# Optimization experiments

Hardware: AMD Instinct MI355X
Metric: run time of the kernel (lower is better)

## Reference

```python
import jax, jax.numpy as jnp
import numpy as np

B, N, E, H = 8, 512, 256, 8
HD = E // H
FF = 4 * E
TOPK = max(1, int(N * 0.2))
FW_MAX_DIST = 10      # default of get_shortest_path_matrix
EMB_MAX_IDX = 6       # spd encoder: max_dist(5) + 1
LN_EPS = 1e-5


def _layernorm(x, g, b):
    m = jnp.mean(x, axis=-1, keepdims=True)
    v = jnp.var(x, axis=-1, keepdims=True)
    return (x - m) / jnp.sqrt(v + LN_EPS) * g + b


def setup_inputs() -> dict:
    key = jax.random.key(0)
    ks = jax.random.split(key, 12)
    s = 0.02
    return {
        "x": jax.random.normal(ks[0], (B, N, E), jnp.float32),
        "adj": jax.random.uniform(ks[1], (B, N, N), jnp.float32),
        "emb_spd": (jax.random.normal(ks[2], (EMB_MAX_IDX + 1, H), jnp.float32) * s),
        "w_qkv": jax.random.normal(ks[3], (3 * E, E), jnp.float32) * s,
        "b_qkv": jnp.zeros((3 * E,), jnp.float32),
        "w_out": jax.random.normal(ks[4], (E, E), jnp.float32) * s,
        "b_out": jnp.zeros((E,), jnp.float32),
        "w_ff1": jax.random.normal(ks[5], (FF, E), jnp.float32) * s,
        "b_ff1": jnp.zeros((FF,), jnp.float32),
        "w_ff2": jax.random.normal(ks[6], (E, FF), jnp.float32) * s,
        "b_ff2": jnp.zeros((E,), jnp.float32),
        "g1": jnp.ones((E,), jnp.float32),
        "beta1": jnp.zeros((E,), jnp.float32),
        "g2": jnp.ones((E,), jnp.float32),
        "beta2": jnp.zeros((E,), jnp.float32),
        "w_pool": jax.random.normal(ks[7], (1, E), jnp.float32) * s,
        "b_pool": jnp.zeros((1,), jnp.float32),
    }


def _combined_mask(adj, emb_spd):
    # top-k per row -> binary adjacency via scatter
    _, idx = jax.lax.top_k(adj, TOPK)                       # [B,N,k]
    bi = jnp.arange(B)[:, None, None]
    ri = jnp.arange(N)[None, :, None]
    binary = jnp.zeros_like(adj).at[bi, ri, idx].set(1.0)   # [B,N,N]

    # Floyd-Warshall shortest paths
    dist = jnp.where(binary == 1.0, 1.0, jnp.inf)
    ids = jnp.arange(N)
    dist = dist.at[:, ids, ids].set(0.0)

    def body(k, d):
        return jnp.minimum(d, d[:, :, k][:, :, None] + d[:, k, :][:, None, :])

    dist = jax.lax.fori_loop(0, N, body, dist)
    dist_i = jnp.where(dist > FW_MAX_DIST, -1.0, dist).astype(jnp.int32)

    # spatial bias embedding: indices = clamp(dist+1, 0, max_dist+1)
    sp_idx = jnp.clip(dist_i + 1, 0, EMB_MAX_IDX)           # [B,N,N]
    bias = jnp.transpose(emb_spd[sp_idx], (0, 3, 1, 2))     # [B,H,N,N]

    base = jnp.where(binary == 0.0, -jnp.inf, 0.0)[:, None] # [B,1,N,N]
    return base + bias                                      # [B,H,N,N]


def reference(x, adj, emb_spd, w_qkv, b_qkv, w_out, b_out,
              w_ff1, b_ff1, w_ff2, b_ff2, g1, beta1, g2, beta2,
              w_pool, b_pool):
    mask = _combined_mask(adj, emb_spd)                     # [B,H,N,N]

    # multi-head self-attention (PyTorch MHA, post-norm encoder layer, eval)
    qkv = x @ w_qkv.T + b_qkv                               # [B,N,3E]
    q, k, v = jnp.split(qkv, 3, axis=-1)
    q = q.reshape(B, N, H, HD).transpose(0, 2, 1, 3)
    k = k.reshape(B, N, H, HD).transpose(0, 2, 1, 3)
    v = v.reshape(B, N, H, HD).transpose(0, 2, 1, 3)
    scores = jnp.einsum("bhqd,bhkd->bhqk", q, k) / np.sqrt(HD) + mask
    attn = jax.nn.softmax(scores, axis=-1)
    ctx = jnp.einsum("bhqk,bhkd->bhqd", attn, v)
    ctx = ctx.transpose(0, 2, 1, 3).reshape(B, N, E)
    attn_out = ctx @ w_out.T + b_out

    x1 = _layernorm(x + attn_out, g1, beta1)
    ff = jax.nn.relu(x1 @ w_ff1.T + b_ff1) @ w_ff2.T + b_ff2
    x2 = _layernorm(x1 + ff, g2, beta2)

    # attention pooling over nodes
    w = jax.nn.softmax(jnp.tanh(x2 @ w_pool.T + b_pool), axis=1)  # [B,N,1]
    return jnp.sum(x2 * w, axis=1)                          # [B,E]
```

## Files before the change

### kernel.cpp

```cpp
#include <hip/hip_runtime.h>
#include <math.h>


#define B_ 8
#define N_ 512
#define E_ 256
#define H_ 8
#define HD_ 32
#define TOPK_ 102

typedef __attribute__((ext_vector_type(8))) short bf16x8;
typedef __attribute__((ext_vector_type(4))) float f32x4;

__device__ __forceinline__ unsigned short f2b(float f) {
  unsigned u = __builtin_bit_cast(unsigned, f);
  return (unsigned short)((u + 0x7FFFu + ((u >> 16) & 1u)) >> 16);
}

__global__ __launch_bounds__(256) void cvt_all(
    const float* __restrict__ x, const float* __restrict__ wqkv,
    const float* __restrict__ wout, const float* __restrict__ wff1,
    const float* __restrict__ wff2, unsigned short* __restrict__ xb,
    unsigned short* __restrict__ wqkvb, unsigned short* __restrict__ woutb,
    unsigned short* __restrict__ wff1b, unsigned short* __restrict__ wff2b) {
  int i = (blockIdx.x * 256 + threadIdx.x) * 4;
  const float* src;
  unsigned short* dst;
  int off;
  if (i < 1048576)      { src = x;    dst = xb;    off = i; }
  else if (i < 1245184) { src = wqkv; dst = wqkvb; off = i - 1048576; }
  else if (i < 1310720) { src = wout; dst = woutb; off = i - 1245184; }
  else if (i < 1572864) { src = wff1; dst = wff1b; off = i - 1310720; }
  else                  { src = wff2; dst = wff2b; off = i - 1572864; }
  float4 v = *(const float4*)(src + off);
  ushort4 o;
  o.x = f2b(v.x); o.y = f2b(v.y); o.z = f2b(v.z); o.w = f2b(v.w);
  *(ushort4*)(dst + off) = o;
}

__global__ __launch_bounds__(256) void topk_kernel(const float* __restrict__ adj,
                                                   unsigned int* __restrict__ bits) {
  const int row = blockIdx.x;
  const float* a = adj + (size_t)row * N_;
  __shared__ unsigned int hist[1024];
  __shared__ float cval[N_];
  __shared__ int cidx[N_];
  __shared__ int s_cnt;
  __shared__ int s_bb;
  __shared__ int s_need;
  __shared__ unsigned int rowbits[16];
  __shared__ int wsum[4];
  const int t = threadIdx.x;
  const int lane = t & 63;
  const int wave = t >> 6;

  hist[t] = 0u; hist[t + 256] = 0u; hist[t + 512] = 0u; hist[t + 768] = 0u;
  if (t == 0) s_cnt = 0;
  float v0 = a[t];
  float v1 = a[t + 256];
  __syncthreads();
  const int b0 = min(1023, max(0, (int)(v0 * 1024.0f)));
  const int b1 = min(1023, max(0, (int)(v1 * 1024.0f)));
  atomicAdd(&hist[b0], 1u);
  atomicAdd(&hist[b1], 1u);
  __syncthreads();
  const int base = 1020 - 4 * t;
  const int h0 = (int)hist[base], h1 = (int)hist[base + 1];
  const int h2 = (int)hist[base + 2], h3 = (int)hist[base + 3];
  const int g = h0 + h1 + h2 + h3;
  int sc = g;
  #pragma unroll
  for (int off = 1; off < 64; off <<= 1) {
    int y = __shfl_up(sc, off);
    sc += (lane >= off) ? y : 0;
  }
  if (lane == 63) wsum[wave] = sc;
  __syncthreads();
  int wo = 0;
  for (int w = 0; w < wave; w++) wo += wsum[w];
  const int incl = sc + wo;
  const int excl = incl - g;
  if (excl < TOPK_ && incl >= TOPK_) {
    int cum = excl;
    int bb = base;
    const int hh[4] = {h3, h2, h1, h0};
    const int bs[4] = {base + 3, base + 2, base + 1, base};
    #pragma unroll
    for (int u = 0; u < 4; u++) {
      if (cum + hh[u] >= TOPK_) { bb = bs[u]; break; }
      cum += hh[u];
    }
    s_bb = bb;
    s_need = TOPK_ - cum;
  }
  __syncthreads();
  const int bb = s_bb;
  const int need = s_need;
  const bool sel0 = (b0 > bb);
  const bool sel1 = (b1 > bb);
  if (b0 == bb) { int p = atomicAdd(&s_cnt, 1); cval[p] = v0; cidx[p] = t; }
  if (b1 == bb) { int p = atomicAdd(&s_cnt, 1); cval[p] = v1; cidx[p] = t + 256; }
  unsigned long long m0 = __ballot(sel0);
  unsigned long long m1 = __ballot(sel1);
  if (lane == 0) {
    rowbits[2 * wave + 0] = (unsigned int)m0;
    rowbits[2 * wave + 1] = (unsigned int)(m0 >> 32);
    rowbits[8 + 2 * wave + 0] = (unsigned int)m1;
    rowbits[8 + 2 * wave + 1] = (unsigned int)(m1 >> 32);
  }
  __syncthreads();
  const int cnt = s_cnt;
  for (int c = t; c < cnt; c += 256) {
    const float v = cval[c];
    const int idx = cidx[c];
    int r = 0;
    for (int j = 0; j < cnt; j++) {
      const float vj = cval[j];
      const int ij = cidx[j];
      if (vj > v || (vj == v && ij < idx)) r++;
    }
    if (r < need) atomicOr(&rowbits[idx >> 5], 1u << (idx & 31));
  }
  __syncthreads();
  if (t < 16) bits[(size_t)row * 16 + t] = rowbits[t];
}

__global__ __launch_bounds__(256) void gemm_mfma(
    const unsigned short* __restrict__ A, const unsigned short* __restrict__ W,
    const float* __restrict__ bias, const float* __restrict__ res,
    void* __restrict__ Cout, unsigned short* __restrict__ kG,
    unsigned short* __restrict__ vG, int M, int N, int K, int flags) {
  __shared__ __align__(16) unsigned short Af[8 * 64 * 8];
  __shared__ __align__(16) unsigned short Wf[8 * 64 * 8];
  const int tid = threadIdx.x;
  const int m0 = blockIdx.y * 64, n0 = blockIdx.x * 64;
  const int wave = tid >> 6, lane = tid & 63;
  const int wm = wave & 1, wn = wave >> 1;
  const int q = lane >> 4, l15 = lane & 15;
  const int r = tid >> 2, c0 = tid & 3;

  f32x4 acc[2][2];
  #pragma unroll
  for (int i = 0; i < 2; i++)
    #pragma unroll
    for (int j = 0; j < 2; j++) acc[i][j] = (f32x4){0.f, 0.f, 0.f, 0.f};

  const size_t arow = (size_t)(m0 + r) * K;
  const size_t wrow = (size_t)(n0 + r) * K;
  for (int k0 = 0; k0 < K; k0 += 64) {
    uint4 a0 = *(const uint4*)(A + arow + k0 + c0 * 8);
    uint4 a1 = *(const uint4*)(A + arow + k0 + (c0 + 4) * 8);
    uint4 w0 = *(const uint4*)(W + wrow + k0 + c0 * 8);
    uint4 w1 = *(const uint4*)(W + wrow + k0 + (c0 + 4) * 8);
    __syncthreads();
    {
      int kc = c0 >> 2, qq = c0 & 3;
      int s0 = ((r >> 4) * 2 + kc) * 64 + (r & 15) + qq * 16;
      int kc1 = (c0 + 4) >> 2, qq1 = (c0 + 4) & 3;
      int s1 = ((r >> 4) * 2 + kc1) * 64 + (r & 15) + qq1 * 16;
      *(uint4*)(Af + s0 * 8) = a0;
      *(uint4*)(Af + s1 * 8) = a1;
      *(uint4*)(Wf + s0 * 8) = w0;
      *(uint4*)(Wf + s1 * 8) = w1;
    }
    __syncthreads();
    #pragma unroll
    for (int kc = 0; kc < 2; kc++) {
      bf16x8 af[2], wf[2];
      #pragma unroll
      for (int mt = 0; mt < 2; mt++)
        af[mt] = *(const bf16x8*)(Af + (((wm * 2 + mt) * 2 + kc) * 64 + lane) * 8);
      #pragma unroll
      for (int nt = 0; nt < 2; nt++)
        wf[nt] = *(const bf16x8*)(Wf + (((wn * 2 + nt) * 2 + kc) * 64 + lane) * 8);
      #pragma unroll
      for (int mt = 0; mt < 2; mt++)
        #pragma unroll
        for (int nt = 0; nt < 2; nt++)
          acc[mt][nt] = __builtin_amdgcn_mfma_f32_16x16x32_bf16(af[mt], wf[nt], acc[mt][nt], 0, 0, 0);
    }
  }
  #pragma unroll
  for (int nt = 0; nt < 2; nt++) {
    const int col = n0 + (wn * 2 + nt) * 16 + l15;
    const float bv = bias[col];
    #pragma unroll
    for (int mt = 0; mt < 2; mt++) {
      const int rowb = m0 + (wm * 2 + mt) * 16 + q * 4;
      float ov[4];
      #pragma unroll
      for (int reg = 0; reg < 4; reg++) {
        float o = acc[mt][nt][reg] + bv;
        if (res) o += res[(size_t)(rowb + reg) * N + col];
        if (flags & 1) o = fmaxf(o, 0.f);
        ov[reg] = o;
      }
      if (kG && col >= 256 && col < 512) {
        const int dfull = col - 256;
        const int hh2 = dfull >> 5, d = dfull & 31;
        const int q2 = d >> 3, sub = d & 7;
        const int bidx = rowb >> 9, j = rowb & 511;
        const int jt = j >> 6, jtile = (j >> 4) & 3, jl = j & 15;
        unsigned short* kp = kG +
            ((size_t)(((bidx * 8 + hh2) * 8 + jt) * 4 + jtile) * 64 + q2 * 16 + jl) * 8 + sub;
        kp[0] = f2b(ov[0]); kp[8] = f2b(ov[1]); kp[16] = f2b(ov[2]); kp[24] = f2b(ov[3]);
      } else if (vG && col >= 512) {
        const int dfull = col - 512;
        const int hh2 = dfull >> 5, d = dfull & 31;
        const int dt = d >> 4, dl = d & 15;
        const int bidx = rowb >> 9, j = rowb & 511;
        const int jt = j >> 6, jj = j & 63;
        const int kc = jj >> 5, q2 = (jj >> 3) & 3, sub0 = jj & 7;
        ushort4 st;
        st.x = f2b(ov[0]); st.y = f2b(ov[1]); st.z = f2b(ov[2]); st.w = f2b(ov[3]);
        *(ushort4*)(vG +
            ((size_t)(((bidx * 8 + hh2) * 8 + jt) * 4 + dt * 2 + kc) * 64 + q2 * 16 + dl) * 8 + sub0) = st;
      } else {
        #pragma unroll
        for (int reg = 0; reg < 4; reg++) {
          if (flags & 2) ((unsigned short*)Cout)[(size_t)(rowb + reg) * N + col] = f2b(ov[reg]);
          else           ((float*)Cout)[(size_t)(rowb + reg) * N + col] = ov[reg];
        }
      }
    }
  }
}

__global__ __launch_bounds__(256) void attn_mfma(
    const unsigned short* __restrict__ qkv, const unsigned short* __restrict__ kG,
    const unsigned short* __restrict__ vG, const unsigned int* __restrict__ bits,
    const float* __restrict__ emb, unsigned short* __restrict__ ctxo) {
  const int bx = blockIdx.x;
  const int ib = bx & 7;
  const int h = (bx >> 3) & 7;
  const int b = bx >> 6;
  const int tid = threadIdx.x;
  const int lane = tid & 63;
  const int wave = tid >> 6;
  const int q = lane >> 4, l15 = lane & 15;

  __shared__ __align__(16) unsigned int mrow[64 * 16];
  __shared__ __align__(16) unsigned short pF[4][2 * 64 * 8];

  {
    int rr = tid >> 2, wq = tid & 3;
    uint4 mw = *(const uint4*)(bits + ((size_t)(b * N_ + ib * 64 + rr)) * 16 + wq * 4);
    *(uint4*)(mrow + rr * 16 + wq * 4) = mw;
  }
  __syncthreads();

  const int i0w = ib * 64 + wave * 16;
  const bf16x8 qf = *(const bf16x8*)(qkv + ((size_t)(b * N_ + i0w + l15)) * 768 + h * HD_ + q * 8);
  const float delta = emb[1 * H_ + h] - emb[2 * H_ + h];
  const float scale = 0.17677669529663687f;

  float m_run[4], l_run[4];
  #pragma unroll
  for (int e = 0; e < 4; e++) { m_run[e] = -1e30f; l_run[e] = 0.f; }
  f32x4 cacc[2];
  cacc[0] = (f32x4){0.f, 0.f, 0.f, 0.f};
  cacc[1] = (f32x4){0.f, 0.f, 0.f, 0.f};

  unsigned short* pbase = &pF[wave][0];
  const unsigned short* kb = kG + (size_t)(b * 8 + h) * 8 * 4 * 512;
  const unsigned short* vb = vG + (size_t)(b * 8 + h) * 8 * 4 * 512;

  #pragma unroll 1
  for (int jt = 0; jt < 8; jt++) {
    f32x4 s4[4];
    #pragma unroll
    for (int jtile = 0; jtile < 4; jtile++) {
      bf16x8 kf = *(const bf16x8*)(kb + (size_t)(jt * 4 + jtile) * 512 + lane * 8);
      s4[jtile] = __builtin_amdgcn_mfma_f32_16x16x32_bf16(qf, kf, (f32x4){0.f, 0.f, 0.f, 0.f}, 0, 0, 0);
    }
    unsigned long long mw64[4];
    #pragma unroll
    for (int reg = 0; reg < 4; reg++)
      mw64[reg] = *(const unsigned long long*)(mrow + (wave * 16 + q * 4 + reg) * 16 + jt * 2);
    float smat[4][4];
    #pragma unroll
    for (int jtile = 0; jtile < 4; jtile++) {
      #pragma unroll
      for (int reg = 0; reg < 4; reg++) {
        unsigned int w = (jtile & 2) ? (unsigned int)(mw64[reg] >> 32) : (unsigned int)mw64[reg];
        bool allowed = ((w >> ((jtile & 1) * 16 + l15)) & 1u) != 0u;
        int ig = ib * 64 + wave * 16 + q * 4 + reg;
        int jg = jt * 64 + jtile * 16 + l15;
        float s = s4[jtile][reg] * scale + ((jg == ig) ? delta : 0.f);
        smat[jtile][reg] = allowed ? s : -INFINITY;
      }
    }
    float alpha[4], pmat[4][4];
    #pragma unroll
    for (int reg = 0; reg < 4; reg++) {
      float mloc = fmaxf(fmaxf(smat[0][reg], smat[1][reg]), fmaxf(smat[2][reg], smat[3][reg]));
      #pragma unroll
      for (int off = 1; off < 16; off <<= 1) mloc = fmaxf(mloc, __shfl_xor(mloc, off));
      float mnew = fmaxf(m_run[reg], mloc);
      alpha[reg] = __expf(m_run[reg] - mnew);
      m_run[reg] = mnew;
      float ps = 0.f;
      #pragma unroll
      for (int jtile = 0; jtile < 4; jtile++) {
        float p = __expf(smat[jtile][reg] - mnew);
        pmat[jtile][reg] = p;
        ps += p;
      }
      #pragma unroll
      for (int off = 1; off < 16; off <<= 1) ps += __shfl_xor(ps, off);
      l_run[reg] = l_run[reg] * alpha[reg] + ps;
      cacc[0][reg] *= alpha[reg];
      cacc[1][reg] *= alpha[reg];
    }
    #pragma unroll
    for (int jtile = 0; jtile < 4; jtile++) {
      int j_l = jtile * 16 + l15;
      int sl = ((j_l >> 5) * 64 + ((j_l >> 3) & 3) * 16) * 8 + (j_l & 7);
      #pragma unroll
      for (int reg = 0; reg < 4; reg++)
        pbase[sl + (q * 4 + reg) * 8] = f2b(pmat[jtile][reg]);
    }
    #pragma unroll
    for (int kc = 0; kc < 2; kc++) {
      bf16x8 pf = *(const bf16x8*)(pbase + (kc * 64 + lane) * 8);
      #pragma unroll
      for (int dt = 0; dt < 2; dt++) {
        bf16x8 vf = *(const bf16x8*)(vb + (size_t)(jt * 4 + dt * 2 + kc) * 512 + lane * 8);
        cacc[dt] = __builtin_amdgcn_mfma_f32_16x16x32_bf16(pf, vf, cacc[dt], 0, 0, 0);
      }
    }
  }
  #pragma unroll
  for (int reg = 0; reg < 4; reg++) {
    const float linv = 1.f / l_run[reg];
    const size_t row = (size_t)(b * N_ + i0w + q * 4 + reg);
    #pragma unroll
    for (int dt = 0; dt < 2; dt++)
      ctxo[row * E_ + h * HD_ + dt * 16 + l15] = f2b(cacc[dt][reg] * linv);
  }
}

__global__ __launch_bounds__(256) void layernorm_kernel(
    const float* __restrict__ t, const float* __restrict__ g,
    const float* __restrict__ be, float* __restrict__ out,
    unsigned short* __restrict__ outb, const float* __restrict__ wp,
    const float* __restrict__ bp, float* __restrict__ ew) {
  const int row = blockIdx.x;
  const int tid = threadIdx.x;
  float v = t[(size_t)row * E_ + tid];
  float s = v, s2 = v * v;
  #pragma unroll
  for (int off = 32; off > 0; off >>= 1) {
    s += __shfl_xor(s, off);
    s2 += __shfl_xor(s2, off);
  }
  __shared__ float sh[8];
  const int wave = tid >> 6, lane = tid & 63;
  if (lane == 0) { sh[wave] = s; sh[4 + wave] = s2; }
  __syncthreads();
  s = sh[0] + sh[1] + sh[2] + sh[3];
  s2 = sh[4] + sh[5] + sh[6] + sh[7];
  float mean = s * (1.f / 256.f);
  float var = s2 * (1.f / 256.f) - mean * mean;
  float inv = rsqrtf(var + 1e-5f);
  float o = (v - mean) * inv * g[tid] + be[tid];
  out[(size_t)row * E_ + tid] = o;
  if (outb) outb[(size_t)row * E_ + tid] = f2b(o);
  if (ew) {
    float d = o * wp[tid];
    #pragma unroll
    for (int off = 32; off > 0; off >>= 1) d += __shfl_xor(d, off);
    __syncthreads();
    if (lane == 0) sh[wave] = d;
    __syncthreads();
    if (tid == 0) {
      float dot = sh[0] + sh[1] + sh[2] + sh[3] + bp[0];
      ew[row] = __expf(tanhf(dot));
    }
  }
}

__global__ __launch_bounds__(256) void pool_partial(
    const float* __restrict__ x2, const float* __restrict__ ew,
    float* __restrict__ partial, float* __restrict__ pwsum) {
  const int c = blockIdx.x;
  const int b = blockIdx.y;
  const int tid = threadIdx.x;
  const int r0 = b * N_ + c * 16;
  float acc = 0.f;
  #pragma unroll
  for (int n = 0; n < 16; n++)
    acc += ew[r0 + n] * x2[(size_t)(r0 + n) * E_ + tid];
  partial[(size_t)(b * 32 + c) * E_ + tid] = acc;
  if (tid < 16) {
    float w = ew[r0 + tid];
    #pragma unroll
    for (int off = 1; off < 16; off <<= 1) w += __shfl_xor(w, off);
    if (tid == 0) pwsum[b * 32 + c] = w;
  }
}

__global__ __launch_bounds__(256) void pool_final(
    const float* __restrict__ partial, const float* __restrict__ pwsum,
    float* __restrict__ out) {
  const int b = blockIdx.x;
  const int tid = threadIdx.x;
  float acc = 0.f, ws = 0.f;
  #pragma unroll
  for (int c = 0; c < 32; c++) acc += partial[(size_t)(b * 32 + c) * E_ + tid];
  #pragma unroll
  for (int c = 0; c < 32; c++) ws += pwsum[b * 32 + c];
  out[b * E_ + tid] = acc / ws;
}

extern "C" void kernel_launch(void* const* d_in, const int* in_sizes, int n_in,
                              void* d_out, int out_size, void* d_ws, size_t ws_size,
                              hipStream_t stream) {
  (void)in_sizes; (void)n_in; (void)out_size; (void)ws_size;
  const float* x      = (const float*)d_in[0];
  const float* adj    = (const float*)d_in[1];
  const float* emb    = (const float*)d_in[2];
  const float* w_qkv  = (const float*)d_in[3];
  const float* b_qkv  = (const float*)d_in[4];
  const float* w_out  = (const float*)d_in[5];
  const float* b_out  = (const float*)d_in[6];
  const float* w_ff1  = (const float*)d_in[7];
  const float* b_ff1  = (const float*)d_in[8];
  const float* w_ff2  = (const float*)d_in[9];
  const float* b_ff2  = (const float*)d_in[10];
  const float* g1     = (const float*)d_in[11];
  const float* be1    = (const float*)d_in[12];
  const float* g2     = (const float*)d_in[13];
  const float* be2    = (const float*)d_in[14];
  const float* w_pool = (const float*)d_in[15];
  const float* b_pool = (const float*)d_in[16];

  char* ws = (char*)d_ws;
  unsigned int*   bits  = (unsigned int*)ws;
  unsigned short* xb    = (unsigned short*)(ws + 262144);
  unsigned short* qkvb  = (unsigned short*)(ws + 2359296);
  unsigned short* hffb  = xb;
  unsigned short* ctxb  = (unsigned short*)(ws + 8650752);
  unsigned short* x1b   = (unsigned short*)(ws + 10747904);
  unsigned short* wqkvb = (unsigned short*)(ws + 12845056);
  unsigned short* woutb = (unsigned short*)(ws + 13238272);
  unsigned short* wff1b = (unsigned short*)(ws + 13369344);
  unsigned short* wff2b = (unsigned short*)(ws + 13893632);
  unsigned short* vG    = (unsigned short*)(ws + 14417920);
  unsigned short* kG    = (unsigned short*)(ws + 16515072);
  float*          tbuf  = (float*)(ws + 18612224);
  float*          x1    = (float*)(ws + 22806528);
  float*          x2    = (float*)(ws + 27000832);
  float*          ew      = (float*)(ws + 8650752);
  float*          partial = (float*)(ws + 8650752 + 16384);
  float*          pwsum   = (float*)(ws + 8650752 + 16384 + 262144);
  float*          outp  = (float*)d_out;

  const int M = B_ * N_;

  cvt_all<<<1835008 / 1024, 256, 0, stream>>>(x, w_qkv, w_out, w_ff1, w_ff2,
                                              xb, wqkvb, woutb, wff1b, wff2b);
  topk_kernel<<<B_ * N_, 256, 0, stream>>>(adj, bits);
  gemm_mfma<<<dim3(768 / 64, M / 64), 256, 0, stream>>>(
      xb, wqkvb, b_qkv, nullptr, qkvb, kG, vG, M, 768, E_, 2);
  attn_mfma<<<B_ * H_ * (N_ / 64), 256, 0, stream>>>(qkvb, kG, vG, bits, emb, ctxb);
  gemm_mfma<<<dim3(E_ / 64, M / 64), 256, 0, stream>>>(
      ctxb, woutb, b_out, x, tbuf, nullptr, nullptr, M, E_, E_, 0);
  layernorm_kernel<<<M, 256, 0, stream>>>(tbuf, g1, be1, x1, x1b,
                                          nullptr, nullptr, nullptr);
  gemm_mfma<<<dim3(1024 / 64, M / 64), 256, 0, stream>>>(
      x1b, wff1b, b_ff1, nullptr, hffb, nullptr, nullptr, M, 1024, E_, 1 | 2);
  gemm_mfma<<<dim3(E_ / 64, M / 64), 256, 0, stream>>>(
      hffb, wff2b, b_ff2, x1, tbuf, nullptr, nullptr, M, E_, 1024, 0);
  layernorm_kernel<<<M, 256, 0, stream>>>(tbuf, g2, be2, x2, nullptr,
                                          w_pool, b_pool, ew);
  pool_partial<<<dim3(32, 8), 256, 0, stream>>>(x2, ew, partial, pwsum);
  pool_final<<<B_, 256, 0, stream>>>(partial, pwsum, outp);
}
```

Measured before the change: 177.5 us.

## Fuse transformer stages into cooperative persistent megakernel with grid syncs

```diff
diff --git a/kernel.cpp b/kernel.cpp
--- a/kernel.cpp
+++ b/kernel.cpp
@@ -1,4 +1,5 @@
 #include <hip/hip_runtime.h>
+#include <hip/hip_cooperative_groups.h>
 #include <math.h>
 
 
@@ -9,6 +10,8 @@
 #define HD_ 32
 #define TOPK_ 102
 
+namespace cg = cooperative_groups;
+
 typedef __attribute__((ext_vector_type(8))) short bf16x8;
 typedef __attribute__((ext_vector_type(4))) float f32x4;
 
@@ -17,40 +20,53 @@
   return (unsigned short)((u + 0x7FFFu + ((u >> 16) & 1u)) >> 16);
 }
 
-__global__ __launch_bounds__(256) void cvt_all(
+struct SmemGemm { unsigned short Af[8 * 64 * 8]; unsigned short Wf[8 * 64 * 8]; };
+struct SmemAttn { unsigned int mrow[64 * 16]; unsigned short pF[4][2 * 64 * 8]; };
+struct SmemLN   { float red[8]; };
+union SmemU { SmemGemm gm; SmemAttn at; SmemLN ln; };
+
+struct MegaArgs {
+  const unsigned short *xb, *wqkvb, *woutb, *wff1b, *wff2b;
+  const unsigned int* bits;
+  const float *x, *emb, *b_qkv, *b_out, *b_ff1, *b_ff2;
+  const float *g1, *be1, *g2, *be2, *wp, *bp;
+  unsigned short *qb, *kG, *vG, *ctxb, *x1b, *hffb;
+  float *tbuf, *x1, *partial, *pwsum, *outp;
+};
+
+__global__ __launch_bounds__(256) void cvt_topk(
+    const float* __restrict__ adj, unsigned int* __restrict__ bits,
     const float* __restrict__ x, const float* __restrict__ wqkv,
     const float* __restrict__ wout, const float* __restrict__ wff1,
     const float* __restrict__ wff2, unsigned short* __restrict__ xb,
     unsigned short* __restrict__ wqkvb, unsigned short* __restrict__ woutb,
     unsigned short* __restrict__ wff1b, unsigned short* __restrict__ wff2b) {
-  int i = (blockIdx.x * 256 + threadIdx.x) * 4;
-  const float* src;
-  unsigned short* dst;
-  int off;
-  if (i < 1048576)      { src = x;    dst = xb;    off = i; }
-  else if (i < 1245184) { src = wqkv; dst = wqkvb; off = i - 1048576; }
-  else if (i < 1310720) { src = wout; dst = woutb; off = i - 1245184; }
-  else if (i < 1572864) { src = wff1; dst = wff1b; off = i - 1310720; }
-  else                  { src = wff2; dst = wff2b; off = i - 1572864; }
-  float4 v = *(const float4*)(src + off);
-  ushort4 o;
-  o.x = f2b(v.x); o.y = f2b(v.y); o.z = f2b(v.z); o.w = f2b(v.w);
-  *(ushort4*)(dst + off) = o;
-}
-
-__global__ __launch_bounds__(256) void topk_kernel(const float* __restrict__ adj,
-                                                   unsigned int* __restrict__ bits) {
-  const int row = blockIdx.x;
-  const float* a = adj + (size_t)row * N_;
   __shared__ unsigned int hist[1024];
-  __shared__ float cval[N_];
-  __shared__ int cidx[N_];
-  __shared__ int s_cnt;
-  __shared__ int s_bb;
-  __shared__ int s_need;
+  __shared__ float cval[64];
+  __shared__ int cidx[64];
+  __shared__ int s_cnt, s_bb, s_need;
   __shared__ unsigned int rowbits[16];
   __shared__ int wsum[4];
   const int t = threadIdx.x;
+
+  if (blockIdx.x >= 4096) {
+    int i = ((blockIdx.x - 4096) * 256 + t) * 4;
+    const float* src;
+    unsigned short* dst;
+    int off;
+    if (i < 1048576)      { src = x;    dst = xb;    off = i; }
+    else if (i < 1245184) { src = wqkv; dst = wqkvb; off = i - 1048576; }
+    else if (i < 1310720) { src = wout; dst = woutb; off = i - 1245184; }
+    else if (i < 1572864) { src = wff1; dst = wff1b; off = i - 1310720; }
+    else                  { src = wff2; dst = wff2b; off = i - 1572864; }
+    float4 v = *(const float4*)(src + off);
+    ushort4 o;
+    o.x = f2b(v.x); o.y = f2b(v.y); o.z = f2b(v.z); o.w = f2b(v.w);
+    *(ushort4*)(dst + off) = o;
+    return;
+  }
+  const int row = blockIdx.x;
+  const float* a = adj + (size_t)row * N_;
   const int lane = t & 63;
   const int wave = t >> 6;
 
@@ -98,8 +114,8 @@
   const int need = s_need;
   const bool sel0 = (b0 > bb);
   const bool sel1 = (b1 > bb);
-  if (b0 == bb) { int p = atomicAdd(&s_cnt, 1); cval[p] = v0; cidx[p] = t; }
-  if (b1 == bb) { int p = atomicAdd(&s_cnt, 1); cval[p] = v1; cidx[p] = t + 256; }
+  if (b0 == bb) { int p = atomicAdd(&s_cnt, 1); if (p < 64) { cval[p] = v0; cidx[p] = t; } }
+  if (b1 == bb) { int p = atomicAdd(&s_cnt, 1); if (p < 64) { cval[p] = v1; cidx[p] = t + 256; } }
   unsigned long long m0 = __ballot(sel0);
   unsigned long long m1 = __ballot(sel1);
   if (lane == 0) {
@@ -109,7 +125,7 @@
     rowbits[8 + 2 * wave + 1] = (unsigned int)(m1 >> 32);
   }
   __syncthreads();
-  const int cnt = s_cnt;
+  const int cnt = min(s_cnt, 64);
   for (int c = t; c < cnt; c += 256) {
     const float v = cval[c];
     const int idx = cidx[c];
@@ -125,15 +141,15 @@
   if (t < 16) bits[(size_t)row * 16 + t] = rowbits[t];
 }
 
-__global__ __launch_bounds__(256) void gemm_mfma(
+__device__ __forceinline__ void gemm_tile(
+    unsigned short* __restrict__ Af, unsigned short* __restrict__ Wf,
     const unsigned short* __restrict__ A, const unsigned short* __restrict__ W,
     const float* __restrict__ bias, const float* __restrict__ res,
-    void* __restrict__ Cout, unsigned short* __restrict__ kG,
-    unsigned short* __restrict__ vG, int M, int N, int K, int flags) {
-  __shared__ __align__(16) unsigned short Af[8 * 64 * 8];
-  __shared__ __align__(16) unsigned short Wf[8 * 64 * 8];
+    void* __restrict__ Cout, unsigned short* __restrict__ qb,
+    unsigned short* __restrict__ kG, unsigned short* __restrict__ vG,
+    int bx, int by, int N, int K, int flags) {
   const int tid = threadIdx.x;
-  const int m0 = blockIdx.y * 64, n0 = blockIdx.x * 64;
+  const int m0 = by * 64, n0 = bx * 64;
   const int wave = tid >> 6, lane = tid & 63;
   const int wm = wave & 1, wn = wave >> 1;
   const int q = lane >> 4, l15 = lane & 15;
@@ -195,42 +211,51 @@
         if (flags & 1) o = fmaxf(o, 0.f);
         ov[reg] = o;
       }
-      if (kG && col >= 256 && col < 512) {
-        const int dfull = col - 256;
-        const int hh2 = dfull >> 5, d = dfull & 31;
-        const int q2 = d >> 3, sub = d & 7;
-        const int bidx = rowb >> 9, j = rowb & 511;
-        const int jt = j >> 6, jtile = (j >> 4) & 3, jl = j & 15;
-        unsigned short* kp = kG +
-            ((size_t)(((bidx * 8 + hh2) * 8 + jt) * 4 + jtile) * 64 + q2 * 16 + jl) * 8 + sub;
-        kp[0] = f2b(ov[0]); kp[8] = f2b(ov[1]); kp[16] = f2b(ov[2]); kp[24] = f2b(ov[3]);
-      } else if (vG && col >= 512) {
-        const int dfull = col - 512;
-        const int hh2 = dfull >> 5, d = dfull & 31;
-        const int dt = d >> 4, dl = d & 15;
-        const int bidx = rowb >> 9, j = rowb & 511;
-        const int jt = j >> 6, jj = j & 63;
-        const int kc = jj >> 5, q2 = (jj >> 3) & 3, sub0 = jj & 7;
-        ushort4 st;
-        st.x = f2b(ov[0]); st.y = f2b(ov[1]); st.z = f2b(ov[2]); st.w = f2b(ov[3]);
-        *(ushort4*)(vG +
-            ((size_t)(((bidx * 8 + hh2) * 8 + jt) * 4 + dt * 2 + kc) * 64 + q2 * 16 + dl) * 8 + sub0) = st;
+      if (flags & 4) {
+        if (col < 256) {
+          #pragma unroll
+          for (int reg = 0; reg < 4; reg++)
+            qb[(size_t)(rowb + reg) * 256 + col] = f2b(ov[reg]);
+        } else if (col < 512) {
+          const int dfull = col - 256;
+          const int hh2 = dfull >> 5, d = dfull & 31;
+          const int q2 = d >> 3, sub = d & 7;
+          const int bidx = rowb >> 9, j = rowb & 511;
+          const int jt = j >> 6, jtile = (j >> 4) & 3, jl = j & 15;
+          unsigned short* kp = kG +
+              ((size_t)(((bidx * 8 + hh2) * 8 + jt) * 4 + jtile) * 64 + q2 * 16 + jl) * 8 + sub;
+          kp[0] = f2b(ov[0]); kp[8] = f2b(ov[1]); kp[16] = f2b(ov[2]); kp[24] = f2b(ov[3]);
+        } else {
+          const int dfull = col - 512;
+          const int hh2 = dfull >> 5, d = dfull & 31;
+          const int dt = d >> 4, dl = d & 15;
+          const int bidx = rowb >> 9, j = rowb & 511;
+          const int jt = j >> 6, jj = j & 63;
+          const int kc = jj >> 5, q2 = (jj >> 3) & 3, sub0 = jj & 7;
+          ushort4 st;
+          st.x = f2b(ov[0]); st.y = f2b(ov[1]); st.z = f2b(ov[2]); st.w = f2b(ov[3]);
+          *(ushort4*)(vG +
+              ((size_t)(((bidx * 8 + hh2) * 8 + jt) * 4 + dt * 2 + kc) * 64 + q2 * 16 + dl) * 8 + sub0) = st;
+        }
+      } else if (flags & 2) {
+        #pragma unroll
+        for (int reg = 0; reg < 4; reg++)
+          ((unsigned short*)Cout)[(size_t)(rowb + reg) * N + col] = f2b(ov[reg]);
       } else {
         #pragma unroll
-        for (int reg = 0; reg < 4; reg++) {
-          if (flags & 2) ((unsigned short*)Cout)[(size_t)(rowb + reg) * N + col] = f2b(ov[reg]);
-          else           ((float*)Cout)[(size_t)(rowb + reg) * N + col] = ov[reg];
-        }
+        for (int reg = 0; reg < 4; reg++)
+          ((float*)Cout)[(size_t)(rowb + reg) * N + col] = ov[reg];
       }
     }
   }
 }
 
-__global__ __launch_bounds__(256) void attn_mfma(
-    const unsigned short* __restrict__ qkv, const unsigned short* __restrict__ kG,
-    const unsigned short* __restrict__ vG, const unsigned int* __restrict__ bits,
-    const float* __restrict__ emb, unsigned short* __restrict__ ctxo) {
-  const int bx = blockIdx.x;
+__device__ __forceinline__ void attn_tile(
+    unsigned int* __restrict__ mrow, unsigned short* __restrict__ pFb,
+    int bx, const unsigned short* __restrict__ qbuf,
+    const unsigned short* __restrict__ kG, const unsigned short* __restrict__ vG,
+    const unsigned int* __restrict__ bits, const float* __restrict__ emb,
+    unsigned short* __restrict__ ctxo) {
   const int ib = bx & 7;
   const int h = (bx >> 3) & 7;
   const int b = bx >> 6;
@@ -239,9 +264,6 @@
   const int wave = tid >> 6;
   const int q = lane >> 4, l15 = lane & 15;
 
-  __shared__ __align__(16) unsigned int mrow[64 * 16];
-  __shared__ __align__(16) unsigned short pF[4][2 * 64 * 8];
-
   {
     int rr = tid >> 2, wq = tid & 3;
     uint4 mw = *(const uint4*)(bits + ((size_t)(b * N_ + ib * 64 + rr)) * 16 + wq * 4);
@@ -250,7 +272,7 @@
   __syncthreads();
 
   const int i0w = ib * 64 + wave * 16;
-  const bf16x8 qf = *(const bf16x8*)(qkv + ((size_t)(b * N_ + i0w + l15)) * 768 + h * HD_ + q * 8);
+  const bf16x8 qf = *(const bf16x8*)(qbuf + ((size_t)(b * N_ + i0w + l15)) * 256 + h * HD_ + q * 8);
   const float delta = emb[1 * H_ + h] - emb[2 * H_ + h];
   const float scale = 0.17677669529663687f;
 
@@ -261,7 +283,7 @@
   cacc[0] = (f32x4){0.f, 0.f, 0.f, 0.f};
   cacc[1] = (f32x4){0.f, 0.f, 0.f, 0.f};
 
-  unsigned short* pbase = &pF[wave][0];
+  unsigned short* pbase = pFb + wave * 1024;
   const unsigned short* kb = kG + (size_t)(b * 8 + h) * 8 * 4 * 512;
   const unsigned short* vb = vG + (size_t)(b * 8 + h) * 8 * 4 * 512;
 
@@ -340,77 +362,149 @@
   }
 }
 
-__global__ __launch_bounds__(256) void layernorm_kernel(
-    const float* __restrict__ t, const float* __restrict__ g,
-    const float* __restrict__ be, float* __restrict__ out,
-    unsigned short* __restrict__ outb, const float* __restrict__ wp,
-    const float* __restrict__ bp, float* __restrict__ ew) {
-  const int row = blockIdx.x;
+__device__ __forceinline__ void ln_row(
+    float* __restrict__ red, int row, const float* __restrict__ t,
+    const float* __restrict__ g, const float* __restrict__ be,
+    float* __restrict__ xo, unsigned short* __restrict__ xbo) {
   const int tid = threadIdx.x;
-  float v = t[(size_t)row * E_ + tid];
+  const int wave = tid >> 6, lane = tid & 63;
+  float v = t[(size_t)row * 256 + tid];
   float s = v, s2 = v * v;
   #pragma unroll
-  for (int off = 32; off > 0; off >>= 1) {
-    s += __shfl_xor(s, off);
-    s2 += __shfl_xor(s2, off);
-  }
-  __shared__ float sh[8];
-  const int wave = tid >> 6, lane = tid & 63;
-  if (lane == 0) { sh[wave] = s; sh[4 + wave] = s2; }
-  __syncthreads();
-  s = sh[0] + sh[1] + sh[2] + sh[3];
-  s2 = sh[4] + sh[5] + sh[6] + sh[7];
+  for (int off = 32; off > 0; off >>= 1) { s += __shfl_xor(s, off); s2 += __shfl_xor(s2, off); }
+  __syncthreads();
+  if (lane == 0) { red[wave] = s; red[4 + wave] = s2; }
+  __syncthreads();
+  s = red[0] + red[1] + red[2] + red[3];
+  s2 = red[4] + red[5] + red[6] + red[7];
   float mean = s * (1.f / 256.f);
   float var = s2 * (1.f / 256.f) - mean * mean;
   float inv = rsqrtf(var + 1e-5f);
   float o = (v - mean) * inv * g[tid] + be[tid];
-  out[(size_t)row * E_ + tid] = o;
-  if (outb) outb[(size_t)row * E_ + tid] = f2b(o);
-  if (ew) {
-    float d = o * wp[tid];
+  xo[(size_t)row * 256 + tid] = o;
+  xbo[(size_t)row * 256 + tid] = f2b(o);
+}
+
+__device__ __forceinline__ void ln2pool_chunk(
+    float* __restrict__ red, int c, const float* __restrict__ t,
+    const float* __restrict__ g, const float* __restrict__ be,
+    const float* __restrict__ wp, const float* __restrict__ bp,
+    float* __restrict__ partial, float* __restrict__ pwsum) {
+  const int tid = threadIdx.x;
+  const int wave = tid >> 6, lane = tid & 63;
+  const float wpv = wp[tid];
+  float pacc = 0.f, esum = 0.f;
+  #pragma unroll 1
+  for (int rr = 0; rr < 16; rr++) {
+    const int row = c * 16 + rr;
+    float v = t[(size_t)row * 256 + tid];
+    float s = v, s2 = v * v;
+    #pragma unroll
+    for (int off = 32; off > 0; off >>= 1) { s += __shfl_xor(s, off); s2 += __shfl_xor(s2, off); }
+    __syncthreads();
+    if (lane == 0) { red[wave] = s; red[4 + wave] = s2; }
+    __syncthreads();
+    s = red[0] + red[1] + red[2] + red[3];
+    s2 = red[4] + red[5] + red[6] + red[7];
+    float mean = s * (1.f / 256.f);
+    float var = s2 * (1.f / 256.f) - mean * mean;
+    float inv = rsqrtf(var + 1e-5f);
+    float o = (v - mean) * inv * g[tid] + be[tid];
+    float d = o * wpv;
     #pragma unroll
     for (int off = 32; off > 0; off >>= 1) d += __shfl_xor(d, off);
     __syncthreads();
-    if (lane == 0) sh[wave] = d;
+    if (lane == 0) red[wave] = d;
     __syncthreads();
-    if (tid == 0) {
-      float dot = sh[0] + sh[1] + sh[2] + sh[3] + bp[0];
-      ew[row] = __expf(tanhf(dot));
-    }
-  }
-}
-
-__global__ __launch_bounds__(256) void pool_partial(
-    const float* __restrict__ x2, const float* __restrict__ ew,
-    float* __restrict__ partial, float* __restrict__ pwsum) {
-  const int c = blockIdx.x;
-  const int b = blockIdx.y;
+    float dot = red[0] + red[1] + red[2] + red[3] + bp[0];
+    float e = __expf(tanhf(dot));
+    pacc += e * o;
+    esum += e;
+  }
+  partial[(size_t)c * 256 + tid] = pacc;
+  if (tid == 0) pwsum[c] = esum;
+}
+
+__device__ __forceinline__ void pool_final_task(
+    int b, const float* __restrict__ partial, const float* __restrict__ pwsum,
+    float* __restrict__ out) {
   const int tid = threadIdx.x;
-  const int r0 = b * N_ + c * 16;
-  float acc = 0.f;
-  #pragma unroll
-  for (int n = 0; n < 16; n++)
-    acc += ew[r0 + n] * x2[(size_t)(r0 + n) * E_ + tid];
-  partial[(size_t)(b * 32 + c) * E_ + tid] = acc;
-  if (tid < 16) {
-    float w = ew[r0 + tid];
-    #pragma unroll
-    for (int off = 1; off < 16; off <<= 1) w += __shfl_xor(w, off);
-    if (tid == 0) pwsum[b * 32 + c] = w;
-  }
-}
-
-__global__ __launch_bounds__(256) void pool_final(
-    const float* __restrict__ partial, const float* __restrict__ pwsum,
-    float* __restrict__ out) {
-  const int b = blockIdx.x;
-  const int tid = threadIdx.x;
-  float acc = 0.f, ws = 0.f;
-  #pragma unroll
-  for (int c = 0; c < 32; c++) acc += partial[(size_t)(b * 32 + c) * E_ + tid];
-  #pragma unroll
-  for (int c = 0; c < 32; c++) ws += pwsum[b * 32 + c];
-  out[b * E_ + tid] = acc / ws;
+  float acc = 0.f, wsv = 0.f;
+  #pragma unroll
+  for (int c = 0; c < 32; c++) acc += partial[(size_t)(b * 32 + c) * 256 + tid];
+  #pragma unroll
+  for (int c = 0; c < 32; c++) wsv += pwsum[b * 32 + c];
+  out[b * 256 + tid] = acc / wsv;
+}
+
+__global__ __launch_bounds__(256, 2) void mega(MegaArgs a) {
+  cg::grid_group gg = cg::this_grid();
+  __shared__ __align__(16) SmemU sm;
+  const int nb = gridDim.x, bid = blockIdx.x;
+
+  for (int t = bid; t < 768; t += nb)
+    gemm_tile(sm.gm.Af, sm.gm.Wf, a.xb, a.wqkvb, a.b_qkv, nullptr, nullptr,
+              a.qb, a.kG, a.vG, t % 12, t / 12, 768, 256, 4);
+  gg.sync();
+  for (int t = bid; t < 512; t += nb)
+    attn_tile(sm.at.mrow, &sm.at.pF[0][0], t, a.qb, a.kG, a.vG, a.bits, a.emb, a.ctxb);
+  gg.sync();
+  for (int t = bid; t < 256; t += nb)
+    gemm_tile(sm.gm.Af, sm.gm.Wf, a.ctxb, a.woutb, a.b_out, a.x, a.tbuf,
+              nullptr, nullptr, nullptr, t % 4, t / 4, 256, 256, 0);
+  gg.sync();
+  for (int rw = bid; rw < 4096; rw += nb)
+    ln_row(sm.ln.red, rw, a.tbuf, a.g1, a.be1, a.x1, a.x1b);
+  gg.sync();
+  for (int t = bid; t < 1024; t += nb)
+    gemm_tile(sm.gm.Af, sm.gm.Wf, a.x1b, a.wff1b, a.b_ff1, nullptr, a.hffb,
+              nullptr, nullptr, nullptr, t % 16, t / 16, 1024, 256, 1 | 2);
+  gg.sync();
+  for (int t = bid; t < 256; t += nb)
+    gemm_tile(sm.gm.Af, sm.gm.Wf, a.hffb, a.wff2b, a.b_ff2, a.x1, a.tbuf,
+              nullptr, nullptr, nullptr, t % 4, t / 4, 256, 1024, 0);
+  gg.sync();
+  for (int c = bid; c < 256; c += nb)
+    ln2pool_chunk(sm.ln.red, c, a.tbuf, a.g2, a.be2, a.wp, a.bp, a.partial, a.pwsum);
+  gg.sync();
+  for (int b = bid; b < 8; b += nb)
+    pool_final_task(b, a.partial, a.pwsum, a.outp);
+}
+
+__global__ __launch_bounds__(256) void k_qkv(MegaArgs a) {
+  __shared__ __align__(16) SmemGemm g;
+  gemm_tile(g.Af, g.Wf, a.xb, a.wqkvb, a.b_qkv, nullptr, nullptr, a.qb, a.kG, a.vG,
+            blockIdx.x, blockIdx.y, 768, 256, 4);
+}
+__global__ __launch_bounds__(256) void k_attn(MegaArgs a) {
+  __shared__ __align__(16) SmemAttn s;
+  attn_tile(s.mrow, &s.pF[0][0], blockIdx.x, a.qb, a.kG, a.vG, a.bits, a.emb, a.ctxb);
+}
+__global__ __launch_bounds__(256) void k_out(MegaArgs a) {
+  __shared__ __align__(16) SmemGemm g;
+  gemm_tile(g.Af, g.Wf, a.ctxb, a.woutb, a.b_out, a.x, a.tbuf, nullptr, nullptr, nullptr,
+            blockIdx.x, blockIdx.y, 256, 256, 0);
+}
+__global__ __launch_bounds__(256) void k_ln1(MegaArgs a) {
+  __shared__ float red[8];
+  ln_row(red, blockIdx.x, a.tbuf, a.g1, a.be1, a.x1, a.x1b);
+}
+__global__ __launch_bounds__(256) void k_ff1(MegaArgs a) {
+  __shared__ __align__(16) SmemGemm g;
+  gemm_tile(g.Af, g.Wf, a.x1b, a.wff1b, a.b_ff1, nullptr, a.hffb, nullptr, nullptr, nullptr,
+            blockIdx.x, blockIdx.y, 1024, 256, 1 | 2);
+}
+__global__ __launch_bounds__(256) void k_ff2(MegaArgs a) {
+  __shared__ __align__(16) SmemGemm g;
+  gemm_tile(g.Af, g.Wf, a.hffb, a.wff2b, a.b_ff2, a.x1, a.tbuf, nullptr, nullptr, nullptr,
+            blockIdx.x, blockIdx.y, 256, 1024, 0);
+}
+__global__ __launch_bounds__(256) void k_ln2pool(MegaArgs a) {
+  __shared__ float red[8];
+  ln2pool_chunk(red, blockIdx.x, a.tbuf, a.g2, a.be2, a.wp, a.bp, a.partial, a.pwsum);
+}
+__global__ __launch_bounds__(256) void k_poolfinal(MegaArgs a) {
+  pool_final_task(blockIdx.x, a.partial, a.pwsum, a.outp);
 }
 
 extern "C" void kernel_launch(void* const* d_in, const int* in_sizes, int n_in,
@@ -438,42 +532,46 @@
   char* ws = (char*)d_ws;
   unsigned int*   bits  = (unsigned int*)ws;
   unsigned short* xb    = (unsigned short*)(ws + 262144);
-  unsigned short* qkvb  = (unsigned short*)(ws + 2359296);
-  unsigned short* hffb  = xb;
+  unsigned short* qb    = (unsigned short*)(ws + 2359296);
+  unsigned short* kG    = (unsigned short*)(ws + 4456448);
+  unsigned short* vG    = (unsigned short*)(ws + 6553600);
   unsigned short* ctxb  = (unsigned short*)(ws + 8650752);
-  unsigned short* x1b   = (unsigned short*)(ws + 10747904);
-  unsigned short* wqkvb = (unsigned short*)(ws + 12845056);
-  unsigned short* woutb = (unsigned short*)(ws + 13238272);
-  unsigned short* wff1b = (unsigned short*)(ws + 13369344);
-  unsigned short* wff2b = (unsigned short*)(ws + 13893632);
-  unsigned short* vG    = (unsigned short*)(ws + 14417920);
-  unsigned short* kG    = (unsigned short*)(ws + 16515072);
-  float*          tbuf  = (float*)(ws + 18612224);
-  float*          x1    = (float*)(ws + 22806528);
-  float*          x2    = (float*)(ws + 27000832);
-  float*          ew      = (float*)(ws + 8650752);
-  float*          partial = (float*)(ws + 8650752 + 16384);
-  float*          pwsum   = (float*)(ws + 8650752 + 16384 + 262144);
+  float*          tbuf  = (float*)(ws + 10747904);
+  float*          x1    = (float*)(ws + 14942208);
+  unsigned short* x1b   = (unsigned short*)(ws + 19136512);
+  unsigned short* hffb  = (unsigned short*)(ws + 21233664);
+  unsigned short* wqkvb = (unsigned short*)(ws + 29622272);
+  unsigned short* woutb = (unsigned short*)(ws + 30015488);
+  unsigned short* wff1b = (unsigned short*)(ws + 30146560);
+  unsigned short* wff2b = (unsigned short*)(ws + 30670848);
+  float*          partial = (float*)(ws + 31195136);
+  float*          pwsum   = (float*)(ws + 31457280);
   float*          outp  = (float*)d_out;
 
-  const int M = B_ * N_;
-
-  cvt_all<<<1835008 / 1024, 256, 0, stream>>>(x, w_qkv, w_out, w_ff1, w_ff2,
-                                              xb, wqkvb, woutb, wff1b, wff2b);
-  topk_kernel<<<B_ * N_, 256, 0, stream>>>(adj, bits);
-  gemm_mfma<<<dim3(768 / 64, M / 64), 256, 0, stream>>>(
-      xb, wqkvb, b_qkv, nullptr, qkvb, kG, vG, M, 768, E_, 2);
-  attn_mfma<<<B_ * H_ * (N_ / 64), 256, 0, stream>>>(qkvb, kG, vG, bits, emb, ctxb);
-  gemm_mfma<<<dim3(E_ / 64, M / 64), 256, 0, stream>>>(
-      ctxb, woutb, b_out, x, tbuf, nullptr, nullptr, M, E_, E_, 0);
-  layernorm_kernel<<<M, 256, 0, stream>>>(tbuf, g1, be1, x1, x1b,
-                                          nullptr, nullptr, nullptr);
-  gemm_mfma<<<dim3(1024 / 64, M / 64), 256, 0, stream>>>(
-      x1b, wff1b, b_ff1, nullptr, hffb, nullptr, nullptr, M, 1024, E_, 1 | 2);
-  gemm_mfma<<<dim3(E_ / 64, M / 64), 256, 0, stream>>>(
-      hffb, wff2b, b_ff2, x1, tbuf, nullptr, nullptr, M, E_, 1024, 0);
-  layernorm_kernel<<<M, 256, 0, stream>>>(tbuf, g2, be2, x2, nullptr,
-                                          w_pool, b_pool, ew);
-  pool_partial<<<dim3(32, 8), 256, 0, stream>>>(x2, ew, partial, pwsum);
-  pool_final<<<B_, 256, 0, stream>>>(partial, pwsum, outp);
-}
+  cvt_topk<<<4096 + 1792, 256, 0, stream>>>(adj, bits, x, w_qkv, w_out, w_ff1,
+                                            w_ff2, xb, wqkvb, woutb, wff1b, wff2b);
+
+  MegaArgs ma;
+  ma.xb = xb; ma.wqkvb = wqkvb; ma.woutb = woutb; ma.wff1b = wff1b; ma.wff2b = wff2b;
+  ma.bits = bits;
+  ma.x = x; ma.emb = emb; ma.b_qkv = b_qkv; ma.b_out = b_out; ma.b_ff1 = b_ff1;
+  ma.b_ff2 = b_ff2; ma.g1 = g1; ma.be1 = be1; ma.g2 = g2; ma.be2 = be2;
+  ma.wp = w_pool; ma.bp = b_pool;
+  ma.qb = qb; ma.kG = kG; ma.vG = vG; ma.ctxb = ctxb; ma.x1b = x1b; ma.hffb = hffb;
+  ma.tbuf = tbuf; ma.x1 = x1; ma.partial = partial; ma.pwsum = pwsum; ma.outp = outp;
+
+  void* kp[] = {&ma};
+  hipError_t err = hipLaunchCooperativeKernel((void*)mega, dim3(512), dim3(256),
+                                              kp, 0, stream);
+  if (err != hipSuccess) {
+    (void)hipGetLastError();
+    k_qkv<<<dim3(12, 64), 256, 0, stream>>>(ma);
+    k_attn<<<512, 256, 0, stream>>>(ma);
+    k_out<<<dim3(4, 64), 256, 0, stream>>>(ma);
+    k_ln1<<<4096, 256, 0, stream>>>(ma);
+    k_ff1<<<dim3(16, 64), 256, 0, stream>>>(ma);
+    k_ff2<<<dim3(4, 64), 256, 0, stream>>>(ma);
+    k_ln2pool<<<256, 256, 0, stream>>>(ma);
+    k_poolfinal<<<8, 256, 0, stream>>>(ma);
+  }
+}
```

Result: slower. 596.1 us (+235.9%).
